# Kernel tuning notes

Measured on AMD Instinct MI355X. Metric: run time of the kernel, lower is better.

## Reference

```python
import jax, jax.numpy as jnp
import numpy as np

B, P, D, F = 2048, 16, 1024, 512  # batch, n_prompt, dim, fusion_dim
S = 2 * P  # sequence length
H = D // 2  # classifier hidden
LN_EPS = 1e-5


def _ln_relu(y, g, b):
    mu = jnp.mean(y, axis=-1, keepdims=True)
    var = jnp.mean(jnp.square(y - mu), axis=-1, keepdims=True)
    return jax.nn.relu((y - mu) * jax.lax.rsqrt(var + LN_EPS) * g + b)


def setup_inputs() -> dict:
    key = jax.random.key(0)
    ks = jax.random.split(key, 24)
    n = lambda k, shp, scale: jax.random.normal(k, shp, dtype=jnp.float32) * scale
    return {
        "q": n(ks[0], (B, S, D), 1.0),
        # nn.MultiheadAttention (1 head, batch_first)
        "in_proj_w": n(ks[1], (3 * D, D), 1.0 / np.sqrt(D)),
        "in_proj_b": jnp.zeros((3 * D,), jnp.float32),
        "out_w": n(ks[2], (D, D), 1.0 / np.sqrt(D)),
        "out_b": jnp.zeros((D,), jnp.float32),
        # 32 per-position classifiers, stacked: Linear(D,H)+ReLU+Linear(H,1)+ReLU
        "cls_w1": n(ks[3], (S, H, D), 1.0 / np.sqrt(D)),
        "cls_b1": jnp.zeros((S, H), jnp.float32),
        "cls_w2": n(ks[4], (S, H), 1.0 / np.sqrt(H)),
        "cls_b2": jnp.zeros((S,), jnp.float32),
        # fusion / projector heads: Linear(D,F)+LayerNorm(F)+ReLU
        "fus_w": n(ks[5], (F, D), 1.0 / np.sqrt(D)),
        "fus_b": jnp.zeros((F,), jnp.float32),
        "fus_g": jnp.ones((F,), jnp.float32),
        "fus_be": jnp.zeros((F,), jnp.float32),
        "pa_w": n(ks[6], (F, D), 1.0 / np.sqrt(D)),
        "pa_b": jnp.zeros((F,), jnp.float32),
        "pa_g": jnp.ones((F,), jnp.float32),
        "pa_be": jnp.zeros((F,), jnp.float32),
        "pv_w": n(ks[7], (F, D), 1.0 / np.sqrt(D)),
        "pv_b": jnp.zeros((F,), jnp.float32),
        "pv_g": jnp.ones((F,), jnp.float32),
        "pv_be": jnp.zeros((F,), jnp.float32),
    }


def reference(q, in_proj_w, in_proj_b, out_w, out_b,
              cls_w1, cls_b1, cls_w2, cls_b2,
              fus_w, fus_b, fus_g, fus_be,
              pa_w, pa_b, pa_g, pa_be,
              pv_w, pv_b, pv_g, pv_be):
    # --- single-head self-attention (nn.MultiheadAttention, eval mode) ---
    wq, wk, wv = jnp.split(in_proj_w, 3, axis=0)
    bq, bk, bv = jnp.split(in_proj_b, 3, axis=0)
    qp = jnp.einsum('bsd,ed->bse', q, wq) + bq
    kp = jnp.einsum('bsd,ed->bse', q, wk) + bk
    vp = jnp.einsum('bsd,ed->bse', q, wv) + bv
    scores = jnp.einsum('bse,bte->bst', qp, kp) / jnp.sqrt(jnp.float32(D))
    attn = jax.nn.softmax(scores, axis=-1)
    q_att = jnp.einsum('bst,bte->bse', attn, vp)
    q_att = jnp.einsum('bse,de->bsd', q_att, out_w) + out_b

    # --- per-position tiny classifiers, batched over the 32 slots ---
    h = jax.nn.relu(jnp.einsum('bsd,shd->bsh', q, cls_w1) + cls_b1)  # [B,S,H]
    d = jax.nn.relu(jnp.einsum('bsh,sh->bs', h, cls_w2) + cls_b2)    # [B,S]

    d_a = jax.nn.softmax(d[:, :P], axis=-1)
    d_v = jax.nn.softmax(d[:, P:], axis=-1)
    audio = jnp.einsum('bsd,bs->bd', q_att[:, :P, :], d_a)
    video = jnp.einsum('bsd,bs->bd', q_att[:, P:, :], d_v)
    fusion = (audio + video) * 0.5

    fusion_h = _ln_relu(fusion @ fus_w.T + fus_b, fus_g, fus_be)
    fusion_a = _ln_relu(audio @ pa_w.T + pa_b, pa_g, pa_be)
    fusion_v = _ln_relu(video @ pv_w.T + pv_b, pv_g, pv_be)
    return (fusion_h, fusion_a, fusion_v, d_a, d_v)
```

## Files before the change

### kernel.cpp

```cpp
#include <hip/hip_runtime.h>

#define Bdim 2048
#define Sdim 32
#define Ddim 1024
#define Fdim 512
#define Hdim 512

typedef __bf16 bf16_t;
typedef __bf16 bf16x8 __attribute__((ext_vector_type(8)));
typedef __bf16 bf16x4 __attribute__((ext_vector_type(4)));
typedef float  f32x4  __attribute__((ext_vector_type(4)));

#define BM 128
#define BN 128
#define BK 32

__device__ __forceinline__ void gll16(const bf16_t* g, bf16_t* l) {
  __builtin_amdgcn_global_load_lds((const __attribute__((address_space(1))) void*)g,
                                   (__attribute__((address_space(3))) void*)l,
                                   16, 0, 0);
}

__device__ __forceinline__ int swz32(int row, int k) {
  return row * 32 + (((((k >> 3) ^ ((row >> 1) & 3))) << 3) | (k & 7));
}

__global__ void k_cvt_all(const float* __restrict__ q, const float* __restrict__ ipw,
                          const float* __restrict__ ow, const float* __restrict__ cw1,
                          const float* __restrict__ fusw, const float* __restrict__ paw,
                          const float* __restrict__ pvw,
                          bf16_t* __restrict__ q16, bf16_t* __restrict__ w16,
                          bf16_t* __restrict__ ow16, bf16_t* __restrict__ cls16,
                          bf16_t* __restrict__ hw16) {
  long v = (long)blockIdx.x * 256 + threadIdx.x;
  const float* s; bf16_t* d; long off;
  if (v < 16777216L)      { s = q;    d = q16;            off = 0; }
  else if (v < 17563648L) { s = ipw;  d = w16;            off = 16777216L; }
  else if (v < 17825792L) { s = ow;   d = ow16;           off = 17563648L; }
  else if (v < 22020096L) { s = cw1;  d = cls16;          off = 17825792L; }
  else if (v < 22151168L) { s = fusw; d = hw16;           off = 22020096L; }
  else if (v < 22282240L) { s = paw;  d = hw16 + 524288;  off = 22151168L; }
  else                    { s = pvw;  d = hw16 + 1048576; off = 22282240L; }
  long i = (v - off) * 4;
  float4 t = *(const float4*)(s + i);
  bf16x4 o;
  o[0] = (bf16_t)t.x; o[1] = (bf16_t)t.y; o[2] = (bf16_t)t.z; o[3] = (bf16_t)t.w;
  *(bf16x4*)(d + i) = o;
}

__global__ void k_bias_pre(const float* __restrict__ ipw, const float* __restrict__ ipb,
                           const float* __restrict__ ow, const float* __restrict__ ob,
                           float* __restrict__ u, float* __restrict__ w,
                           float* __restrict__ bp, float* __restrict__ c0) {
  int blk = blockIdx.x, tid = threadIdx.x;
  if (blk < 4) {
    int d = blk * 256 + tid;
    float acc = 0.f;
    #pragma unroll 8
    for (int e = 0; e < Ddim; ++e) acc += ipw[(long)e * Ddim + d] * ipb[Ddim + e];
    u[d] = acc;
  } else if (blk < 8) {
    int d = (blk - 4) * 256 + tid;
    float acc = 0.f;
    #pragma unroll 8
    for (int e = 0; e < Ddim; ++e) acc += ipw[(long)(Ddim + e) * Ddim + d] * ipb[e];
    w[d] = acc;
  } else if (blk < 136) {
    int o = (blk - 8) * 8 + (tid >> 5);
    int l = tid & 31;
    float acc = 0.f;
    #pragma unroll 4
    for (int e = l; e < Ddim; e += 32) acc += ow[(long)o * Ddim + e] * ipb[2 * Ddim + e];
    #pragma unroll
    for (int m = 1; m < 32; m <<= 1) acc += __shfl_xor(acc, m);
    if (l == 0) bp[o] = acc + ob[o];
  } else {
    __shared__ float red[256];
    float acc = 0.f;
    for (int e = tid; e < Ddim; e += 256) acc += ipb[e] * ipb[Ddim + e];
    red[tid] = acc;
    __syncthreads();
    for (int off = 128; off; off >>= 1) {
      if (tid < off) red[tid] += red[tid + off];
      __syncthreads();
    }
    if (tid == 0) c0[0] = red[0];
  }
}

template<int AT, int BT>
__device__ __forceinline__ void gemm_tile(const bf16_t* __restrict__ A, long lda,
                                          const bf16_t* __restrict__ Bt, long ldb,
                                          long m0, long n0, int K,
                                          bf16_t* sa, bf16_t* sb, f32x4 acc[4][4]) {
  const int tid  = threadIdx.x;
  const int wave = tid >> 6;
  const int lane = tid & 63;
  const int quad = lane >> 4;
  const int l16  = lane & 15;
  const int wm = (wave & 1) * 64;
  const int wn = (wave >> 1) * 64;

  for (int kt = 0; kt < K; kt += BK) {
    __syncthreads();
    if constexpr (AT == 0) {
      #pragma unroll
      for (int r = 0; r < 2; ++r) {
        int L = r * 256 + tid;
        int row = L >> 2, cs = L & 3;
        int csrc = cs ^ ((row >> 1) & 3);
        gll16(A + (m0 + row) * lda + kt + csrc * 8, sa + (long)(r * 256 + wave * 64) * 8);
      }
    } else {
      #pragma unroll
      for (int r = 0; r < 2; ++r) {
        int L = r * 256 + tid;
        int gk = L >> 4, gm = (L & 15) * 8;
        bf16x8 v = *(const bf16x8*)(A + (long)(kt + gk) * lda + m0 + gm);
        #pragma unroll
        for (int j = 0; j < 8; ++j) sa[swz32(gm + j, gk)] = v[j];
      }
    }
    if constexpr (BT == 0) {
      #pragma unroll
      for (int r = 0; r < 2; ++r) {
        int L = r * 256 + tid;
        int row = L >> 2, cs = L & 3;
        int csrc = cs ^ ((row >> 1) & 3);
        gll16(Bt + (n0 + row) * ldb + kt + csrc * 8, sb + (long)(r * 256 + wave * 64) * 8);
      }
    } else {
      #pragma unroll
      for (int r = 0; r < 2; ++r) {
        int L = r * 256 + tid;
        int gk = L >> 4, gn = (L & 15) * 8;
        bf16x8 v = *(const bf16x8*)(Bt + (long)(kt + gk) * ldb + n0 + gn);
        #pragma unroll
        for (int j = 0; j < 8; ++j) sb[swz32(gn + j, gk)] = v[j];
      }
    }
    __syncthreads();
    bf16x8 af[4], bfr[4];
    #pragma unroll
    for (int i = 0; i < 4; ++i) {
      int row = wm + i * 16 + l16;
      af[i] = *(const bf16x8*)(sa + row * 32 + ((quad ^ ((row >> 1) & 3)) << 3));
    }
    #pragma unroll
    for (int j = 0; j < 4; ++j) {
      int row = wn + j * 16 + l16;
      bfr[j] = *(const bf16x8*)(sb + row * 32 + ((quad ^ ((row >> 1) & 3)) << 3));
    }
    #pragma unroll
    for (int i = 0; i < 4; ++i)
      #pragma unroll
      for (int j = 0; j < 4; ++j)
        acc[i][j] = __builtin_amdgcn_mfma_f32_16x16x32_bf16(bfr[j], af[i], acc[i][j], 0, 0, 0);
  }
}

template<int AT, int BT>
__global__ __launch_bounds__(256) void k_gemm_bf16(
    const bf16_t* __restrict__ A, long lda, long sAz,
    const bf16_t* __restrict__ Bt, long ldb, long sBz,
    bf16_t* __restrict__ C, long ldc, long sCz,
    const float* __restrict__ bias, int K) {
  __shared__ bf16_t sa[BM * BK];
  __shared__ bf16_t sb[BN * BK];
  long n0 = (long)blockIdx.x * BN;
  long m0 = (long)blockIdx.y * BM;
  long z  = blockIdx.z;
  const bf16_t* Az = A + z * sAz;
  const bf16_t* Bz = Bt + z * sBz;
  bf16_t* Cz = C + z * sCz;
  f32x4 acc[4][4];
  #pragma unroll
  for (int i = 0; i < 4; ++i)
    #pragma unroll
    for (int j = 0; j < 4; ++j) acc[i][j] = (f32x4){0.f, 0.f, 0.f, 0.f};
  gemm_tile<AT, BT>(Az, lda, Bz, ldb, m0, n0, K, sa, sb, acc);
  const int tid = threadIdx.x, wave = tid >> 6, lane = tid & 63;
  const int quad = lane >> 4, l16 = lane & 15;
  const int wm = (wave & 1) * 64, wn = (wave >> 1) * 64;
  #pragma unroll
  for (int i = 0; i < 4; ++i) {
    long row = m0 + wm + i * 16 + l16;
    #pragma unroll
    for (int j = 0; j < 4; ++j) {
      long col = n0 + wn + j * 16 + quad * 4;
      f32x4 b4 = bias ? *(const f32x4*)(bias + col) : (f32x4){0.f, 0.f, 0.f, 0.f};
      bf16x4 o;
      #pragma unroll
      for (int r = 0; r < 4; ++r) o[r] = (bf16_t)(acc[i][j][r] + b4[r]);
      *(bf16x4*)(Cz + row * ldc + col) = o;
    }
  }
}

__global__ __launch_bounds__(256) void k_gemm_f32(
    const bf16_t* __restrict__ A, long lda, long sAz,
    const bf16_t* __restrict__ Bt, long ldb, long sBz,
    float* __restrict__ C, long ldc, long sCz, int K) {
  __shared__ bf16_t sa[BM * BK];
  __shared__ bf16_t sb[BN * BK];
  long n0 = (long)blockIdx.x * BN;
  long m0 = (long)blockIdx.y * BM;
  long z  = blockIdx.z;
  const bf16_t* Az = A + z * sAz;
  const bf16_t* Bz = Bt + z * sBz;
  float* Cz = C + z * sCz;
  f32x4 acc[4][4];
  #pragma unroll
  for (int i = 0; i < 4; ++i)
    #pragma unroll
    for (int j = 0; j < 4; ++j) acc[i][j] = (f32x4){0.f, 0.f, 0.f, 0.f};
  gemm_tile<0, 0>(Az, lda, Bz, ldb, m0, n0, K, sa, sb, acc);
  const int tid = threadIdx.x, wave = tid >> 6, lane = tid & 63;
  const int quad = lane >> 4, l16 = lane & 15;
  const int wm = (wave & 1) * 64, wn = (wave >> 1) * 64;
  #pragma unroll
  for (int i = 0; i < 4; ++i) {
    long row = m0 + wm + i * 16 + l16;
    #pragma unroll
    for (int j = 0; j < 4; ++j) {
      long col = n0 + wn + j * 16 + quad * 4;
      *(f32x4*)(Cz + row * ldc + col) = acc[i][j];
    }
  }
}

__global__ __launch_bounds__(512, 2) void k_gemm_big(
    const bf16_t* __restrict__ A, const bf16_t* __restrict__ Bt,
    bf16_t* __restrict__ C) {
  __shared__ bf16_t sa[3][256 * 32];
  __shared__ bf16_t sb[3][256 * 32];
  const int tid = threadIdx.x, wave = tid >> 6, lane = tid & 63;
  const int quad = lane >> 4, l16 = lane & 15;
  int lin = blockIdx.x;
  int c = lin & 7, t0 = lin >> 3;
  int wg = c * 128 + t0;
  long m0 = (long)(wg >> 2) * 256;
  long n0 = (long)(wg & 3) * 256;
  const int wm = (wave >> 2) * 128;
  const int wn = (wave & 3) * 64;
  const int rowS = tid >> 2, cs = tid & 3;
  const int csrcS = cs ^ ((rowS >> 1) & 3);
  const bf16_t* Abase = A + (m0 + rowS) * 1024 + csrcS * 8;
  const bf16_t* Bbase = Bt + (n0 + rowS) * 1024 + csrcS * 8;
  const int dst0 = wave * 512;
  const int dst1 = 4096 + wave * 512;

  f32x4 acc[8][4];
  #pragma unroll
  for (int i = 0; i < 8; ++i)
    #pragma unroll
    for (int j = 0; j < 4; ++j) acc[i][j] = (f32x4){0.f, 0.f, 0.f, 0.f};

#define GB_STAGE(KT, BUF)                                    \
  do {                                                       \
    const bf16_t* Ab = Abase + (KT);                         \
    const bf16_t* Bb = Bbase + (KT);                         \
    gll16(Ab,              sa[BUF] + dst0);                  \
    gll16(Ab + 128 * 1024, sa[BUF] + dst1);                  \
    gll16(Bb,              sb[BUF] + dst0);                  \
    gll16(Bb + 128 * 1024, sb[BUF] + dst1);                  \
  } while (0)

#define GB_COMPUTE(BUF)                                                            \
  do {                                                                             \
    bf16x8 af[8], bfr[4];                                                          \
    _Pragma("unroll")                                                              \
    for (int i = 0; i < 8; ++i) {                                                  \
      int row = wm + i * 16 + l16;                                                 \
      af[i] = *(const bf16x8*)(&sa[BUF][row * 32 + ((quad ^ ((row >> 1) & 3)) << 3)]); \
    }                                                                              \
    _Pragma("unroll")                                                              \
    for (int j = 0; j < 4; ++j) {                                                  \
      int row = wn + j * 16 + l16;                                                 \
      bfr[j] = *(const bf16x8*)(&sb[BUF][row * 32 + ((quad ^ ((row >> 1) & 3)) << 3)]); \
    }                                                                              \
    __builtin_amdgcn_s_setprio(1);                                                 \
    _Pragma("unroll")                                                              \
    for (int i = 0; i < 8; ++i)                                                    \
      _Pragma("unroll")                                                            \
      for (int j = 0; j < 4; ++j)                                                  \
        acc[i][j] = __builtin_amdgcn_mfma_f32_16x16x32_bf16(bfr[j], af[i], acc[i][j], 0, 0, 0); \
    __builtin_amdgcn_s_setprio(0);                                                 \
  } while (0)

#define GB_SYNC(N)                                           \
  asm volatile("s_waitcnt vmcnt(" #N ")" ::: "memory");      \
  __builtin_amdgcn_s_barrier();                              \
  asm volatile("" ::: "memory")

  GB_STAGE(0, 0);
  GB_STAGE(32, 1);

  int kt = 64;
  #pragma unroll 1
  for (int g = 0; g < 10; ++g) {
    GB_SYNC(4);
    GB_STAGE(kt, 2);
    GB_COMPUTE(0);
    GB_SYNC(4);
    GB_STAGE(kt + 32, 0);
    GB_COMPUTE(1);
    GB_SYNC(4);
    GB_STAGE(kt + 64, 1);
    GB_COMPUTE(2);
    kt += 96;
  }
  GB_SYNC(4);
  GB_COMPUTE(0);
  GB_SYNC(0);
  GB_COMPUTE(1);

#undef GB_STAGE
#undef GB_COMPUTE
#undef GB_SYNC

  #pragma unroll
  for (int i = 0; i < 8; ++i) {
    long row = m0 + wm + i * 16 + l16;
    #pragma unroll
    for (int j = 0; j < 4; ++j) {
      long col = n0 + wn + j * 16 + quad * 4;
      bf16x4 o;
      #pragma unroll
      for (int r = 0; r < 4; ++r) o[r] = (bf16_t)(acc[i][j][r]);
      *(bf16x4*)(C + row * 1024 + col) = o;
    }
  }
}

__global__ __launch_bounds__(256) void k_gemm_cls(
    const bf16_t* __restrict__ q16, const bf16_t* __restrict__ w1,
    const float* __restrict__ b1, const float* __restrict__ w2,
    float* __restrict__ dsum) {
  __shared__ bf16_t sa[BM * BK];
  __shared__ bf16_t sb[BN * BK];
  int lin = ((int)blockIdx.z * 16 + blockIdx.y) * 4 + blockIdx.x;
  int c = lin & 7, j0 = lin >> 3;
  int p = c + 8 * (j0 >> 2);
  long n0 = (long)(j0 & 3) * BN;
  int s = p >> 4;
  long m0 = (long)(p & 15) * BM;
  const bf16_t* A  = q16 + (long)s * Ddim;
  const bf16_t* Bt = w1 + (long)s * Hdim * Ddim;
  f32x4 acc[4][4];
  #pragma unroll
  for (int i = 0; i < 4; ++i)
    #pragma unroll
    for (int j = 0; j < 4; ++j) acc[i][j] = (f32x4){0.f, 0.f, 0.f, 0.f};
  gemm_tile<0, 0>(A, (long)Sdim * Ddim, Bt, Ddim, m0, n0, Ddim, sa, sb, acc);
  const int tid = threadIdx.x, wave = tid >> 6, lane = tid & 63;
  const int quad = lane >> 4, l16 = lane & 15;
  const int wm = (wave & 1) * 64, wn = (wave >> 1) * 64;
  const float* b1s = b1 + (long)s * Hdim;
  const float* w2s = w2 + (long)s * Hdim;
  #pragma unroll
  for (int i = 0; i < 4; ++i) {
    float vsum = 0.f;
    #pragma unroll
    for (int j = 0; j < 4; ++j) {
      long col = n0 + wn + j * 16 + quad * 4;
      f32x4 b4 = *(const f32x4*)(b1s + col);
      f32x4 w4 = *(const f32x4*)(w2s + col);
      #pragma unroll
      for (int r = 0; r < 4; ++r)
        vsum += fmaxf(acc[i][j][r] + b4[r], 0.f) * w4[r];
    }
    vsum += __shfl_xor(vsum, 16);
    vsum += __shfl_xor(vsum, 32);
    if (lane < 16) {
      long row = m0 + wm + i * 16 + l16;
      atomicAdd(&dsum[row * Sdim + s], vsum);
    }
  }
}

__global__ void k_finalize_d(const float* __restrict__ dsum, const float* __restrict__ cb2,
                             float* __restrict__ daws, float* __restrict__ out_da,
                             float* __restrict__ out_dv) {
  int t = blockIdx.x * 256 + threadIdx.x;
  int b = t >> 5, s = t & 31;
  float v = fmaxf(dsum[t] + cb2[s], 0.f);
  float m = v;
  #pragma unroll
  for (int mask = 1; mask < 16; mask <<= 1) m = fmaxf(m, __shfl_xor(m, mask));
  float e = __expf(v - m);
  float sum = e;
  #pragma unroll
  for (int mask = 1; mask < 16; mask <<= 1) sum += __shfl_xor(sum, mask);
  float r = e / sum;
  daws[t] = r;
  if (s < 16) out_da[b * 16 + s] = r;
  else        out_dv[b * 16 + (s - 16)] = r;
}

#define QPAD 264
__global__ __launch_bounds__(256) void k_attn_pool(
    const bf16_t* __restrict__ q16, const bf16_t* __restrict__ G16,
    const float* __restrict__ daws, const float* __restrict__ u,
    const float* __restrict__ wv, const float* __restrict__ c0p,
    bf16_t* __restrict__ pooled) {
  __shared__ bf16_t qc[32 * QPAD];
  __shared__ bf16_t gc[32 * QPAD];
  __shared__ float sc[32][33];
  __shared__ float qup[32][8], qwp[32][8];
  __shared__ float quL[32], qwL[32], caL[32], cvL[32], daL[16], dvL[16];
  const int tid = threadIdx.x, wave = tid >> 6, lane = tid & 63;
  const int quad = lane >> 4, l16 = lane & 15;
  const long b = blockIdx.x;
  const bf16_t* qb = q16 + b * (Sdim * Ddim);
  const bf16_t* gb = G16 + b * (Sdim * Ddim);
  if (tid < 32) {
    float dval = daws[b * Sdim + tid];
    if (tid < 16) daL[tid] = dval; else dvL[tid - 16] = dval;
  }
  qup[tid >> 3][tid & 7] = 0.f;
  qwp[tid >> 3][tid & 7] = 0.f;
  const int ti = wave & 1, tj = wave >> 1;
  f32x4 acc = (f32x4){0.f, 0.f, 0.f, 0.f};
  for (int kc = 0; kc < Ddim; kc += 256) {
    __syncthreads();
    #pragma unroll
    for (int r = 0; r < 4; ++r) {
      int L = r * 256 + tid;
      int row = L >> 5, koff = (L & 31) * 8;
      *(bf16x8*)(qc + row * QPAD + koff) = *(const bf16x8*)(qb + (long)row * Ddim + kc + koff);
      *(bf16x8*)(gc + row * QPAD + koff) = *(const bf16x8*)(gb + (long)row * Ddim + kc + koff);
    }
    __syncthreads();
    #pragma unroll
    for (int kk = 0; kk < 8; ++kk) {
      bf16x8 a  = *(const bf16x8*)(gc + (ti * 16 + l16) * QPAD + kk * 32 + quad * 8);
      bf16x8 bb = *(const bf16x8*)(qc + (tj * 16 + l16) * QPAD + kk * 32 + quad * 8);
      acc = __builtin_amdgcn_mfma_f32_16x16x32_bf16(a, bb, acc, 0, 0, 0);
    }
    {
      int s2 = tid & 31, sl = tid >> 5;
      float pu = 0.f, pw = 0.f;
      const bf16_t* qrow = qc + s2 * QPAD + sl * 32;
      const float* ub = u + kc + sl * 32;
      const float* wb = wv + kc + sl * 32;
      #pragma unroll
      for (int kb = 0; kb < 4; ++kb) {
        bf16x8 qv = *(const bf16x8*)(qrow + kb * 8);
        f32x4 u0 = *(const f32x4*)(ub + kb * 8);
        f32x4 u1 = *(const f32x4*)(ub + kb * 8 + 4);
        f32x4 w0 = *(const f32x4*)(wb + kb * 8);
        f32x4 w1 = *(const f32x4*)(wb + kb * 8 + 4);
        #pragma unroll
        for (int e = 0; e < 4; ++e) {
          pu += (float)qv[e] * u0[e] + (float)qv[e + 4] * u1[e];
          pw += (float)qv[e] * w0[e] + (float)qv[e + 4] * w1[e];
        }
      }
      qup[s2][sl] += pu;
      qwp[s2][sl] += pw;
    }
  }
  __syncthreads();
  if (tid < 32) {
    float a0 = 0.f, a1 = 0.f;
    for (int k = 0; k < 8; ++k) { a0 += qup[tid][k]; a1 += qwp[tid][k]; }
    quL[tid] = a0; qwL[tid] = a1;
  }
  __syncthreads();
  {
    float c00 = c0p[0];
    int col = tj * 16 + l16;
    #pragma unroll
    for (int r = 0; r < 4; ++r) {
      int row = ti * 16 + quad * 4 + r;
      sc[row][col] = (acc[r] + quL[row] + qwL[col] + c00) * 0.03125f;
    }
  }
  __syncthreads();
  if (tid < 32) {
    float mx = -1e30f;
    for (int t = 0; t < 32; ++t) mx = fmaxf(mx, sc[tid][t]);
    float sum = 0.f;
    for (int t = 0; t < 32; ++t) { float e = __expf(sc[tid][t] - mx); sc[tid][t] = e; sum += e; }
    float inv = 1.f / sum;
    for (int t = 0; t < 32; ++t) sc[tid][t] *= inv;
  }
  __syncthreads();
  if (tid < 32) {
    float a0 = 0.f, a1 = 0.f;
    for (int s2 = 0; s2 < 16; ++s2) a0 += daL[s2] * sc[s2][tid];
    for (int s2 = 0; s2 < 16; ++s2) a1 += dvL[s2] * sc[16 + s2][tid];
    caL[tid] = a0; cvL[tid] = a1;
  }
  __syncthreads();
  {
    int d0 = tid * 4;
    float ap[4] = {0.f, 0.f, 0.f, 0.f}, vp[4] = {0.f, 0.f, 0.f, 0.f};
    for (int t = 0; t < 32; ++t) {
      float ca = caL[t], cv = cvL[t];
      bf16x4 qv = *(const bf16x4*)(qb + (long)t * Ddim + d0);
      #pragma unroll
      for (int e = 0; e < 4; ++e) {
        float x = (float)qv[e];
        ap[e] += ca * x;
        vp[e] += cv * x;
      }
    }
    bf16x4 pf, pa, pv;
    #pragma unroll
    for (int e = 0; e < 4; ++e) {
      pf[e] = (bf16_t)(0.5f * (ap[e] + vp[e]));
      pa[e] = (bf16_t)ap[e];
      pv[e] = (bf16_t)vp[e];
    }
    *(bf16x4*)(pooled + b * 3072 + d0)        = pf;
    *(bf16x4*)(pooled + b * 3072 + 1024 + d0) = pa;
    *(bf16x4*)(pooled + b * 3072 + 2048 + d0) = pv;
  }
}

__global__ __launch_bounds__(256) void k_ln(
    const float* __restrict__ Y,
    const float* __restrict__ fb, const float* __restrict__ fg, const float* __restrict__ fbe,
    const float* __restrict__ ab, const float* __restrict__ ag, const float* __restrict__ abe,
    const float* __restrict__ vb, const float* __restrict__ vg, const float* __restrict__ vbe,
    float* __restrict__ out) {
  int wave = threadIdx.x >> 6, lane = threadIdx.x & 63;
  long row = (long)blockIdx.x * 4 + wave;
  int head = (int)(row >> 11);
  const float* bb = (head == 0) ? fb : (head == 1) ? ab : vb;
  const float* gg = (head == 0) ? fg : (head == 1) ? ag : vg;
  const float* be = (head == 0) ? fbe : (head == 1) ? abe : vbe;
  const float* y = Y + row * Fdim + lane * 8;
  float v[8];
  float s = 0.f;
  #pragma unroll
  for (int k = 0; k < 8; ++k) { v[k] = y[k] + bb[lane * 8 + k]; s += v[k]; }
  #pragma unroll
  for (int m = 1; m < 64; m <<= 1) s += __shfl_xor(s, m);
  float mu = s * (1.f / Fdim);
  float vs = 0.f;
  #pragma unroll
  for (int k = 0; k < 8; ++k) { float t = v[k] - mu; vs += t * t; }
  #pragma unroll
  for (int m = 1; m < 64; m <<= 1) vs += __shfl_xor(vs, m);
  float inv = rsqrtf(vs * (1.f / Fdim) + 1e-5f);
  float* o = out + row * Fdim + lane * 8;
  #pragma unroll
  for (int k = 0; k < 8; ++k) {
    float t = (v[k] - mu) * inv * gg[lane * 8 + k] + be[lane * 8 + k];
    o[k] = fmaxf(t, 0.f);
  }
}

extern "C" void kernel_launch(void* const* d_in, const int* in_sizes, int n_in,
                              void* d_out, int out_size, void* d_ws, size_t ws_size,
                              hipStream_t stream) {
  const float* q    = (const float*)d_in[0];
  const float* ipw  = (const float*)d_in[1];
  const float* ipb  = (const float*)d_in[2];
  const float* ow   = (const float*)d_in[3];
  const float* ob   = (const float*)d_in[4];
  const float* cw1  = (const float*)d_in[5];
  const float* cb1  = (const float*)d_in[6];
  const float* cw2  = (const float*)d_in[7];
  const float* cb2  = (const float*)d_in[8];
  const float* fusw = (const float*)d_in[9];
  const float* fusb = (const float*)d_in[10];
  const float* fusg = (const float*)d_in[11];
  const float* fusbe= (const float*)d_in[12];
  const float* paw  = (const float*)d_in[13];
  const float* pab  = (const float*)d_in[14];
  const float* pag  = (const float*)d_in[15];
  const float* pabe = (const float*)d_in[16];
  const float* pvw  = (const float*)d_in[17];
  const float* pvb  = (const float*)d_in[18];
  const float* pvg  = (const float*)d_in[19];
  const float* pvbe = (const float*)d_in[20];
  float* out = (float*)d_out;

  const size_t o_q16   = 0;
  const size_t o_w16   = 134217728;
  const size_t o_ow16  = 140509184;
  const size_t o_cls16 = 142606336;
  const size_t o_hw16  = 176160768;
  const size_t o_Mt    = 179306496;
  const size_t o_Nt    = 181403648;
  const size_t o_G16   = 183500800;
  const size_t o_pool  = 317718528;
  const size_t o_u     = 330301440;
  const size_t o_wv    = 330305536;
  const size_t o_bp    = 330309632;
  const size_t o_c0    = 330313728;
  const size_t o_dsum  = 330313984;
  const size_t o_daws  = 330576128;
  const size_t total   = 330838272;
  if (ws_size < total) return;

  char* ws = (char*)d_ws;
  bf16_t* q16   = (bf16_t*)(ws + o_q16);
  bf16_t* w16   = (bf16_t*)(ws + o_w16);
  bf16_t* Wq16  = w16;
  bf16_t* Wk16  = w16 + 1048576;
  bf16_t* Wv16  = w16 + 2097152;
  bf16_t* ow16  = (bf16_t*)(ws + o_ow16);
  bf16_t* cls16 = (bf16_t*)(ws + o_cls16);
  bf16_t* hw16  = (bf16_t*)(ws + o_hw16);
  bf16_t* Mt    = (bf16_t*)(ws + o_Mt);
  bf16_t* Nt    = (bf16_t*)(ws + o_Nt);
  bf16_t* G16   = (bf16_t*)(ws + o_G16);
  bf16_t* S116  = (bf16_t*)(ws + o_G16);
  float*  Yf    = (float*)(ws + o_G16 + 12582912);
  bf16_t* pool16= (bf16_t*)(ws + o_pool);
  float*  uf    = (float*)(ws + o_u);
  float*  wvf   = (float*)(ws + o_wv);
  float*  bpf   = (float*)(ws + o_bp);
  float*  c0f   = (float*)(ws + o_c0);
  float*  dsum  = (float*)(ws + o_dsum);
  float*  daws  = (float*)(ws + o_daws);

  k_cvt_all<<<dim3(87552), dim3(256), 0, stream>>>(
      q, ipw, ow, cw1, fusw, paw, pvw, q16, w16, ow16, cls16, hw16);

  k_bias_pre<<<dim3(137), dim3(256), 0, stream>>>(ipw, ipb, ow, ob, uf, wvf, bpf, c0f);

  k_gemm_bf16<1, 1><<<dim3(8, 8, 1), dim3(256), 0, stream>>>(
      Wk16, Ddim, 0, Wq16, Ddim, 0, Mt, Ddim, 0, nullptr, Ddim);

  k_gemm_bf16<0, 1><<<dim3(8, 8, 1), dim3(256), 0, stream>>>(
      ow16, Ddim, 0, Wv16, Ddim, 0, Nt, Ddim, 0, nullptr, Ddim);

  k_gemm_big<<<dim3(1024), dim3(512), 0, stream>>>(q16, Mt, G16);

  hipMemsetAsync(dsum, 0, (size_t)Bdim * Sdim * sizeof(float), stream);
  k_gemm_cls<<<dim3(4, 16, 32), dim3(256), 0, stream>>>(q16, cls16, cb1, cw2, dsum);

  k_finalize_d<<<dim3(256), dim3(256), 0, stream>>>(
      dsum, cb2, daws, out + 3145728, out + 3145728 + 32768);

  k_attn_pool<<<dim3(2048), dim3(256), 0, stream>>>(q16, G16, daws, uf, wvf, c0f, pool16);

  k_gemm_bf16<0, 0><<<dim3(8, 48, 1), dim3(256), 0, stream>>>(
      pool16, Ddim, 0, Nt, Ddim, 0, S116, Ddim, 0, bpf, Ddim);

  k_gemm_f32<<<dim3(4, 16, 3), dim3(256), 0, stream>>>(
      S116, 3L * Ddim, Ddim, hw16, Ddim, (long)Fdim * Ddim,
      Yf, Fdim, (long)Bdim * Fdim, Ddim);

  k_ln<<<dim3(1536), dim3(256), 0, stream>>>(
      Yf, fusb, fusg, fusbe, pab, pag, pabe, pvb, pvg, pvbe, out);
}
```

Baseline: 1.043 ms.

## Restructure big GEMM into BK=64 double-buffered, phase-interleaved load/MFMA schedule

Replaces the triple-buffered BK=32 main GEMM with a double-buffered BK=64 kernel. Each K tile is split into four phases that interleave quarter-tile global-to-LDS loads with 16-MFMA compute clusters, separated by explicit barriers and sched_barriers. The aim is to hide memory latency and cut barrier frequency per FLOP. In exchange it uses more LDS per block and issues redundant prefetch loads past the end of K on the final iteration.

```diff
diff --git a/kernel.cpp b/kernel.cpp
--- a/kernel.cpp
+++ b/kernel.cpp
@@ -229,11 +229,11 @@
   }
 }
 
-__global__ __launch_bounds__(512, 2) void k_gemm_big(
+__global__ __launch_bounds__(512, 2) void k_gemm_big8(
     const bf16_t* __restrict__ A, const bf16_t* __restrict__ Bt,
     bf16_t* __restrict__ C) {
-  __shared__ bf16_t sa[3][256 * 32];
-  __shared__ bf16_t sb[3][256 * 32];
+  __shared__ bf16_t sa[2][256 * 64];
+  __shared__ bf16_t sb[2][256 * 64];
   const int tid = threadIdx.x, wave = tid >> 6, lane = tid & 63;
   const int quad = lane >> 4, l16 = lane & 15;
   int lin = blockIdx.x;
@@ -243,12 +243,16 @@
   long n0 = (long)(wg & 3) * 256;
   const int wm = (wave >> 2) * 128;
   const int wn = (wave & 3) * 64;
-  const int rowS = tid >> 2, cs = tid & 3;
-  const int csrcS = cs ^ ((rowS >> 1) & 3);
-  const bf16_t* Abase = A + (m0 + rowS) * 1024 + csrcS * 8;
-  const bf16_t* Bbase = Bt + (n0 + rowS) * 1024 + csrcS * 8;
-  const int dst0 = wave * 512;
-  const int dst1 = 4096 + wave * 512;
+
+  const int csA = tid & 7;
+  const bf16_t* aSrc = A + (m0 + (tid >> 3)) * 1024 + (long)((csA ^ ((tid >> 4) & 7)) * 8);
+  const int t2 = tid & 255;
+  const bf16_t* bSrc = Bt + (n0 + (t2 >> 3)) * 1024 + (long)(((t2 & 7) ^ ((t2 >> 4) & 7)) * 8);
+
+  const int swzk0 = ((0 * 4 + quad) ^ (l16 >> 1)) << 3;
+  const int swzk1 = ((1 * 4 + quad) ^ (l16 >> 1)) << 3;
+  const int aBase = (wm + l16) * 64;
+  const int bBase = (wn + l16) * 64;
 
   f32x4 acc[8][4];
   #pragma unroll
@@ -256,68 +260,101 @@
     #pragma unroll
     for (int j = 0; j < 4; ++j) acc[i][j] = (f32x4){0.f, 0.f, 0.f, 0.f};
 
-#define GB_STAGE(KT, BUF)                                    \
-  do {                                                       \
-    const bf16_t* Ab = Abase + (KT);                         \
-    const bf16_t* Bb = Bbase + (KT);                         \
-    gll16(Ab,              sa[BUF] + dst0);                  \
-    gll16(Ab + 128 * 1024, sa[BUF] + dst1);                  \
-    gll16(Bb,              sb[BUF] + dst0);                  \
-    gll16(Bb + 128 * 1024, sb[BUF] + dst1);                  \
+  bf16x8 afc[8], bfr0[4], bfr1[4];
+
+#define ST_AQ(SB, KT, Q) \
+  gll16(aSrc + (long)(Q) * 65536 + (KT), &sa[SB][(Q) * 4096 + wave * 512])
+#define ST_BP(SB, KT, OA, OB) do {                                             \
+    int oct_ = (wave < 4) ? (OA) : (OB);                                       \
+    gll16(bSrc + (long)oct_ * 32768 + (KT),                                    \
+          &sb[SB][oct_ * 2048 + (wave & 3) * 512]);                            \
   } while (0)
 
-#define GB_COMPUTE(BUF)                                                            \
-  do {                                                                             \
-    bf16x8 af[8], bfr[4];                                                          \
-    _Pragma("unroll")                                                              \
-    for (int i = 0; i < 8; ++i) {                                                  \
-      int row = wm + i * 16 + l16;                                                 \
-      af[i] = *(const bf16x8*)(&sa[BUF][row * 32 + ((quad ^ ((row >> 1) & 3)) << 3)]); \
-    }                                                                              \
-    _Pragma("unroll")                                                              \
-    for (int j = 0; j < 4; ++j) {                                                  \
-      int row = wn + j * 16 + l16;                                                 \
-      bfr[j] = *(const bf16x8*)(&sb[BUF][row * 32 + ((quad ^ ((row >> 1) & 3)) << 3)]); \
-    }                                                                              \
-    __builtin_amdgcn_s_setprio(1);                                                 \
-    _Pragma("unroll")                                                              \
-    for (int i = 0; i < 8; ++i)                                                    \
-      _Pragma("unroll")                                                            \
-      for (int j = 0; j < 4; ++j)                                                  \
-        acc[i][j] = __builtin_amdgcn_mfma_f32_16x16x32_bf16(bfr[j], af[i], acc[i][j], 0, 0, 0); \
-    __builtin_amdgcn_s_setprio(0);                                                 \
+#define LD_AF(CB, MH) do {                                                     \
+    _Pragma("unroll")                                                          \
+    for (int i = 0; i < 4; ++i) {                                              \
+      afc[i * 2 + 0] = *(const bf16x8*)(&sa[CB][aBase + (MH) * 4096 + i * 1024 + swzk0]); \
+      afc[i * 2 + 1] = *(const bf16x8*)(&sa[CB][aBase + (MH) * 4096 + i * 1024 + swzk1]); \
+    } } while (0)
+#define LD_BF(CB, NH, DST) do {                                                \
+    _Pragma("unroll")                                                          \
+    for (int jj = 0; jj < 2; ++jj) {                                           \
+      DST[jj * 2 + 0] = *(const bf16x8*)(&sb[CB][bBase + (NH) * 2048 + jj * 1024 + swzk0]); \
+      DST[jj * 2 + 1] = *(const bf16x8*)(&sb[CB][bBase + (NH) * 2048 + jj * 1024 + swzk1]); \
+    } } while (0)
+
+#define MFMA16(BF, IOFF, JOFF) do {                                            \
+    __builtin_amdgcn_s_setprio(1);                                             \
+    _Pragma("unroll")                                                          \
+    for (int i = 0; i < 4; ++i)                                                \
+      _Pragma("unroll")                                                        \
+      for (int jj = 0; jj < 2; ++jj)                                           \
+        _Pragma("unroll")                                                      \
+        for (int kh = 0; kh < 2; ++kh)                                         \
+          acc[(IOFF) + i][(JOFF) + jj] = __builtin_amdgcn_mfma_f32_16x16x32_bf16( \
+              BF[jj * 2 + kh], afc[i * 2 + kh], acc[(IOFF) + i][(JOFF) + jj], 0, 0, 0); \
+    __builtin_amdgcn_s_setprio(0);                                             \
+    __builtin_amdgcn_sched_barrier(0);                                         \
   } while (0)
 
-#define GB_SYNC(N)                                           \
-  asm volatile("s_waitcnt vmcnt(" #N ")" ::: "memory");      \
-  __builtin_amdgcn_s_barrier();                              \
-  asm volatile("" ::: "memory")
-
-  GB_STAGE(0, 0);
-  GB_STAGE(32, 1);
-
-  int kt = 64;
+#define BAR1() do {                                                            \
+    asm volatile("" ::: "memory");                                             \
+    __builtin_amdgcn_s_barrier();                                              \
+    asm volatile("s_waitcnt lgkmcnt(0)" ::: "memory");                         \
+    __builtin_amdgcn_sched_barrier(0);                                         \
+  } while (0)
+#define BAR2V() do {                                                           \
+    asm volatile("s_waitcnt vmcnt(4)" ::: "memory");                           \
+    __builtin_amdgcn_s_barrier();                                              \
+    asm volatile("" ::: "memory");                                             \
+  } while (0)
+#define BAR2() do {                                                            \
+    asm volatile("" ::: "memory");                                             \
+    __builtin_amdgcn_s_barrier();                                              \
+    asm volatile("" ::: "memory");                                             \
+  } while (0)
+
+#define TILE(CB, SB, KT2) do {                                                 \
+                                                    \
+    LD_AF(CB, 0); LD_BF(CB, 0, bfr0);                                          \
+    ST_AQ(SB, KT2, 0); ST_AQ(SB, KT2, 2);                                      \
+    BAR1(); MFMA16(bfr0, 0, 0); BAR2V();                                       \
+                                                    \
+    LD_BF(CB, 1, bfr1);                                                        \
+    ST_BP(SB, KT2, 0, 4); ST_BP(SB, KT2, 2, 6);                                \
+    BAR1(); MFMA16(bfr1, 0, 2); BAR2V();                                       \
+                                                    \
+    LD_AF(CB, 1);                                                              \
+    ST_BP(SB, KT2, 1, 5); ST_BP(SB, KT2, 3, 7);                                \
+    BAR1(); MFMA16(bfr1, 4, 2); BAR2();                                        \
+              \
+    ST_AQ(SB, KT2, 1); ST_AQ(SB, KT2, 3);                                      \
+    BAR1(); MFMA16(bfr0, 4, 0); BAR2V();                                       \
+  } while (0)
+
+  ST_AQ(0, 0, 0); ST_AQ(0, 0, 2);
+  ST_BP(0, 0, 0, 4); ST_BP(0, 0, 2, 6);
+  ST_BP(0, 0, 1, 5); ST_BP(0, 0, 3, 7);
+  ST_AQ(0, 0, 1); ST_AQ(0, 0, 3);
+  BAR2V();
+
   #pragma unroll 1
-  for (int g = 0; g < 10; ++g) {
-    GB_SYNC(4);
-    GB_STAGE(kt, 2);
-    GB_COMPUTE(0);
-    GB_SYNC(4);
-    GB_STAGE(kt + 32, 0);
-    GB_COMPUTE(1);
-    GB_SYNC(4);
-    GB_STAGE(kt + 64, 1);
-    GB_COMPUTE(2);
-    kt += 96;
-  }
-  GB_SYNC(4);
-  GB_COMPUTE(0);
-  GB_SYNC(0);
-  GB_COMPUTE(1);
-
-#undef GB_STAGE
-#undef GB_COMPUTE
-#undef GB_SYNC
+  for (int x = 0; x < 16; x += 2) {
+    int ktA = (x + 1) * 64;
+    int ktB = (x + 2) * 64;
+    TILE(0, 1, ktA);
+    TILE(1, 0, ktB);
+  }
+
+#undef ST_AQ
+#undef ST_BP
+#undef LD_AF
+#undef LD_BF
+#undef MFMA16
+#undef BAR1
+#undef BAR2V
+#undef BAR2
+#undef TILE
 
   #pragma unroll
   for (int i = 0; i < 8; ++i) {
@@ -631,7 +668,7 @@
   k_gemm_bf16<0, 1><<<dim3(8, 8, 1), dim3(256), 0, stream>>>(
       ow16, Ddim, 0, Wv16, Ddim, 0, Nt, Ddim, 0, nullptr, Ddim);
 
-  k_gemm_big<<<dim3(1024), dim3(512), 0, stream>>>(q16, Mt, G16);
+  k_gemm_big8<<<dim3(1024), dim3(512), 0, stream>>>(q16, Mt, G16);
 
   hipMemsetAsync(dsum, 0, (size_t)Bdim * Sdim * sizeof(float), stream);
   k_gemm_cls<<<dim3(4, 16, 32), dim3(256), 0, stream>>>(q16, cls16, cb1, cw2, dsum);
```

Result: no change. 1.033 ms (-1.0%).
